# Optimization experiments

Measured on AMD Instinct MI355X. Metric: run time of the kernel, lower is better.

Reference implementation:

```python
import jax, jax.numpy as jnp
import numpy as np

N_NODES = 100000
N_EDGES = 1600000
N_FEAT = 64
HID = 64
HL = 256
N_GRAPHS = 512


def _lin(k, i, o):
    return (jax.random.normal(k, (i, o), jnp.float32) / np.sqrt(i)).astype(jnp.float32)


def setup_inputs() -> dict:
    key = jax.random.key(0)
    ks = jax.random.split(key, 20)
    inp = {
        "x": jax.random.normal(ks[0], (N_NODES, N_FEAT), jnp.float32),
        "edge_index": jax.random.randint(ks[1], (2, N_EDGES), 0, N_NODES),
        "batch": jnp.sort(jax.random.randint(ks[2], (N_NODES,), 0, N_GRAPHS)),
        "T": jax.random.normal(ks[3], (N_GRAPHS, 1), jnp.float32),
    }
    dims = [(N_FEAT, HID), (HID, HID), (HID, HID), (HID, HID)]
    for i, (di, do) in enumerate(dims):
        inp[f"wrel{i}"] = _lin(ks[4 + 3 * i], di, do)
        inp[f"brel{i}"] = jnp.zeros((do,), jnp.float32)
        inp[f"wroot{i}"] = _lin(ks[5 + 3 * i], di, do)
    inp["w1"] = _lin(ks[16], 3 * HID + 1, HL)
    inp["b1"] = jnp.zeros((HL,), jnp.float32)
    inp["w2"] = _lin(ks[17], HL, HL)
    inp["b2"] = jnp.zeros((HL,), jnp.float32)
    inp["w3"] = _lin(ks[18], HL, 1)
    inp["b3"] = jnp.zeros((1,), jnp.float32)
    return inp


def reference(x, edge_index, batch, T,
              wrel0, brel0, wroot0,
              wrel1, brel1, wroot1,
              wrel2, brel2, wroot2,
              wrel3, brel3, wroot3,
              w1, b1, w2, b2, w3, b3):
    src, dst = edge_index[0], edge_index[1]

    def conv(h, wr, br, wq):
        # PyG GraphConv: W_root h_i + W_rel * sum_{j->i} h_j + b_rel
        agg = jax.ops.segment_sum(h[src], dst, num_segments=N_NODES)
        return agg @ wr + br + h @ wq

    h = jax.nn.relu(conv(x, wrel0, brel0, wroot0))
    h = jax.nn.relu(conv(h, wrel1, brel1, wroot1))
    h = jax.nn.relu(conv(h, wrel2, brel2, wroot2))
    h = conv(h, wrel3, brel3, wroot3)  # no relu on conv2 (matches original)

    # global add / mean / max pools over graph ids
    s = jax.ops.segment_sum(h, batch, num_segments=N_GRAPHS)
    cnt = jax.ops.segment_sum(jnp.ones((N_NODES, 1), h.dtype), batch, num_segments=N_GRAPHS)
    mean = s / jnp.maximum(cnt, 1.0)
    mx = jax.ops.segment_max(h, batch, num_segments=N_GRAPHS)
    mx = jnp.where(jnp.isfinite(mx), mx, 0.0)  # empty segments -> 0

    out = jnp.concatenate([mx, mean, s, T], axis=1)  # [G, 3*HID+1]
    o = jax.nn.relu(out @ w1 + b1)
    o = jax.nn.relu(o @ w2 + b2)  # dropout is identity in eval mode
    return o @ w3 + b3
```

## Files before the change

kernel.cpp:

```cpp
#include <hip/hip_runtime.h>
#include <hip/hip_bf16.h>
#include <math.h>

#define N_NODES 100000
#define N_EDGES 1600000
#define N_FEAT 64
#define HID 64
#define HL 256
#define N_GRAPHS 512

#define BUCKET_BITS 7
#define BUCKET_SIZE 128
#define NB ((N_NODES + BUCKET_SIZE - 1) / BUCKET_SIZE)
#define LOFS_W (NB + 1)
#define CAP 3584
#define LREC_CAP 3584
#define EDGES_PER_BLOCK 4096
#define SCAT_BLOCKS ((N_EDGES + EDGES_PER_BLOCK - 1) / EDGES_PER_BLOCK)
#define F2B_BLOCKS (N_NODES * 16 / 256)
#define WPREP_BLOCKS 128
#define ZOFF ((unsigned int)N_NODES * 128u)
#define FUSE_BLOCKS ((N_NODES + 63) / 64)

typedef short vbf8 __attribute__((ext_vector_type(8)));
typedef float vf4 __attribute__((ext_vector_type(4)));
typedef float vf2 __attribute__((ext_vector_type(2)));
typedef unsigned int vu4 __attribute__((ext_vector_type(4)));

__device__ __forceinline__ unsigned short f2b(float f) {
    unsigned int u = __float_as_uint(f);
    return (unsigned short)((u + 0x7FFFu + ((u >> 16) & 1u)) >> 16);
}
__device__ __forceinline__ float b2f(unsigned short u) {
    return __uint_as_float(((unsigned int)u) << 16);
}
__device__ __forceinline__ unsigned pk2(float lo, float hi) {
    float2 f; f.x = lo; f.y = hi;
    __hip_bfloat162 h = __float22bfloat162_rn(f);
    unsigned r;
    __builtin_memcpy(&r, &h, 4);
    return r;
}
__device__ __forceinline__ vf2 bpair(unsigned int d) {
    vf2 r;
    r.x = __uint_as_float(d << 16);
    r.y = __uint_as_float(d & 0xFFFF0000u);
    return r;
}


__global__ __launch_bounds__(256) void k_mega(
        const int* __restrict__ src, const int* __restrict__ dst,
        int* __restrict__ lofs, unsigned int* __restrict__ ebuf,
        const float4* __restrict__ x, uint2* __restrict__ xb,
        const float* __restrict__ wroot0, const float* __restrict__ wrel0,
        const float* __restrict__ wroot1, const float* __restrict__ wrel1,
        const float* __restrict__ wroot2, const float* __restrict__ wrel2,
        const float* __restrict__ wroot3, const float* __restrict__ wrel3,
        unsigned short* __restrict__ wt) {
    __shared__ int lh[NB];
    __shared__ int lsc[256];
    __shared__ unsigned lrec[EDGES_PER_BLOCK];
    int bid = blockIdx.x;
    int t = threadIdx.x;

    if (bid < SCAT_BLOCKS) {
        for (int i = t; i < NB; i += 256) lh[i] = 0;
        __syncthreads();
        int i0 = bid * EDGES_PER_BLOCK;
        int i1 = min(N_EDGES, i0 + EDGES_PER_BLOCK);
        int cnt = i1 - i0;
        for (int i = i0 + t; i < i1; i += 256)
            atomicAdd(&lh[dst[i] >> BUCKET_BITS], 1);
        __syncthreads();
        int v[4];
        int s = 0;
        int base4 = t * 4;
#pragma unroll
        for (int j = 0; j < 4; j++) {
            v[j] = (base4 + j < NB) ? lh[base4 + j] : 0;
            s += v[j];
        }
        lsc[t] = s;
        __syncthreads();
        for (int off = 1; off < 256; off <<= 1) {
            int xx = lsc[t];
            int y = (t >= off) ? lsc[t - off] : 0;
            __syncthreads();
            lsc[t] = xx + y;
            __syncthreads();
        }
        int run = lsc[t] - s;
        int* lrow = lofs + (size_t)bid * LOFS_W;
#pragma unroll
        for (int j = 0; j < 4; j++) {
            int b = base4 + j;
            if (b < NB) {
                lrow[b] = run;
                lh[b] = run;
            }
            run += v[j];
        }
        if (t == 255) lrow[NB] = cnt;
        __syncthreads();
        for (int i = i0 + t; i < i1; i += 256) {
            int sN = src[i], d = dst[i];
            int b = d >> BUCKET_BITS;
            int p = atomicAdd(&lh[b], 1);
            lrec[p] = ((unsigned)sN << 7) | (unsigned)(d & 127);
        }
        __syncthreads();
        unsigned* eb = ebuf + (size_t)bid * EDGES_PER_BLOCK;
        for (int j = t; j < cnt; j += 256) eb[j] = lrec[j];
    } else if (bid < SCAT_BLOCKS + F2B_BLOCKS) {
        int i = (bid - SCAT_BLOCKS) * 256 + t;
        if (i < N_NODES * 16) {
            float4 v = x[i];
            uint2 o;
            o.x = pk2(v.x, v.y);
            o.y = pk2(v.z, v.w);
            xb[i] = o;
        }
    } else {
        int gi = (bid - SCAT_BLOCKS - F2B_BLOCKS) * 256 + t;
        if (gi < 4 * 64 * 128) {
            int layer = gi >> 13;
            int i = gi & 8191;
            int nn = i >> 7, k = i & 127;
            const float* wr = (layer == 0) ? wroot0 : (layer == 1) ? wroot1
                             : (layer == 2) ? wroot2 : wroot3;
            const float* wl = (layer == 0) ? wrel0 : (layer == 1) ? wrel1
                             : (layer == 2) ? wrel2 : wrel3;
            float v = (k < 64) ? wr[k * 64 + nn] : wl[(k - 64) * 64 + nn];
            wt[gi] = f2b(v);
        }
    }
}


__global__ __launch_bounds__(256) void k_fscatter2(
        const unsigned int* __restrict__ ebuf, const int* __restrict__ lofs,
        int2* __restrict__ re, unsigned int* __restrict__ soff,
        unsigned short* __restrict__ hbA, unsigned short* __restrict__ hbB, int n) {
    __shared__ int rcnt[512];
    __shared__ int rbase[512];
    __shared__ int rpre[512];
    __shared__ int tsc[256];
    __shared__ unsigned lrec[LREC_CAP];
    __shared__ int lcnt[BUCKET_SIZE];
    __shared__ int sc[BUCKET_SIZE];
    __shared__ int cur[BUCKET_SIZE];
    int b = blockIdx.x;
    int n0 = b * BUCKET_SIZE;
    int t = threadIdx.x;
    if (b == 0 && t < 16) {
        uint4 z = make_uint4(0u, 0u, 0u, 0u);
        unsigned short* hp = (t < 8) ? hbA : hbB;
        ((uint4*)(hp + (size_t)N_NODES * 64))[t & 7] = z;
    }
    for (int blk = t; blk < 512; blk += 256) {
        int c = 0, ba = 0;
        if (blk < SCAT_BLOCKS) {
            const int* lr = lofs + (size_t)blk * LOFS_W + b;
            ba = lr[0];
            c = lr[1] - ba;
        }
        rcnt[blk] = c;
        rbase[blk] = ba;
    }
    __syncthreads();
    int c0 = rcnt[2 * t], c1 = rcnt[2 * t + 1];
    tsc[t] = c0 + c1;
    __syncthreads();
    for (int off = 1; off < 256; off <<= 1) {
        int xx = tsc[t];
        int y = (t >= off) ? tsc[t - off] : 0;
        __syncthreads();
        tsc[t] = xx + y;
        __syncthreads();
    }
    int ex = tsc[t] - (c0 + c1);
    rpre[2 * t] = ex;
    rpre[2 * t + 1] = ex + c0;
    __syncthreads();
    int cb = tsc[255];
    for (int blk = t; blk < SCAT_BLOCKS; blk += 256) {
        int c = rcnt[blk];
        int dsto = rpre[blk];
        const unsigned* sp = ebuf + (size_t)blk * EDGES_PER_BLOCK + rbase[blk];
        for (int j = 0; j < c; j++) lrec[dsto + j] = sp[j];
    }
    if (t < BUCKET_SIZE) lcnt[t] = 0;
    __syncthreads();
    for (int r = t; r < cb; r += 256)
        atomicAdd(&lcnt[lrec[r] & 127u], 1);
    __syncthreads();
    int v = 0, pcnt = 0;
    if (t < BUCKET_SIZE) {
        v = lcnt[t];
        pcnt = (v + 7) & ~7;
        sc[t] = pcnt;
    }
    __syncthreads();
    for (int off = 1; off < BUCKET_SIZE; off <<= 1) {
        int xx = 0;
        if (t < BUCKET_SIZE) {
            xx = sc[t];
            if (t >= off) xx += sc[t - off];
        }
        __syncthreads();
        if (t < BUCKET_SIZE) sc[t] = xx;
        __syncthreads();
    }
    if (t < BUCKET_SIZE) {
        int start = b * CAP + sc[t] - pcnt;
        if (n0 + t < n) re[n0 + t] = make_int2(start, start + v);
        cur[t] = start;
        for (int z = start + v; z < start + pcnt; z++) soff[z] = ZOFF;
    }
    __syncthreads();
    for (int r = t; r < cb; r += 256) {
        unsigned rec = lrec[r];
        int p = atomicAdd(&cur[rec & 127u], 1);
        soff[p] = rec & ~127u;
    }
}


template <int RELU>
__global__ __launch_bounds__(512) void k_layer(
    const unsigned short* __restrict__ hb,
    const unsigned short* __restrict__ wt, const float* __restrict__ brel,
    unsigned short* __restrict__ hbout,
    const int2* __restrict__ re, const unsigned int* __restrict__ soff, int n) {
    __shared__ float scx[4][16 * 68];
    __shared__ unsigned int agg_lds[64][32];

    int tid = threadIdx.x;
    int w = tid >> 6, l = tid & 63;
    int r0 = blockIdx.x * 64;

    {
        int g = l >> 3;
        int sl = l & 7;
        int nl = w * 8 + g;
        int i = r0 + nl;
        int ii = min(i, n - 1);
        int2 bd = re[ii];
        int e0 = bd.x;
        int cnt = (i < n) ? (bd.y - bd.x) : 0;
        int pc4 = (cnt + 3) & ~3;
        const char* base = (const char*)hb + sl * 16;

        vf2 A[4], B[4];
#pragma unroll
        for (int f = 0; f < 4; f++) { A[f] = (vf2){0.f, 0.f}; B[f] = (vf2){0.f, 0.f}; }

        for (int it = 0; it < pc4; it += 4) {
            vu4 ov = __builtin_nontemporal_load((const vu4*)(soff + e0 + it));
            uint4 d0 = *(const uint4*)(base + ov.x);
            uint4 d1 = *(const uint4*)(base + ov.y);
            uint4 d2 = *(const uint4*)(base + ov.z);
            uint4 d3 = *(const uint4*)(base + ov.w);
            A[0] += bpair(d0.x); A[1] += bpair(d0.y);
            A[2] += bpair(d0.z); A[3] += bpair(d0.w);
            B[0] += bpair(d1.x); B[1] += bpair(d1.y);
            B[2] += bpair(d1.z); B[3] += bpair(d1.w);
            A[0] += bpair(d2.x); A[1] += bpair(d2.y);
            A[2] += bpair(d2.z); A[3] += bpair(d2.w);
            B[0] += bpair(d3.x); B[1] += bpair(d3.y);
            B[2] += bpair(d3.z); B[3] += bpair(d3.w);
        }

        vf2 s0 = A[0] + B[0];
        vf2 s1 = A[1] + B[1];
        vf2 s2 = A[2] + B[2];
        vf2 s3 = A[3] + B[3];
        uint4 o;
        o.x = pk2(s0.x, s0.y);
        o.y = pk2(s1.x, s1.y);
        o.z = pk2(s2.x, s2.y);
        o.w = pk2(s3.x, s3.y);
        int c16 = sl ^ (nl & 7);
        *(uint4*)&agg_lds[nl][c16 * 4] = o;
    }
    __syncthreads();

    if (w < 4) {
        int lm = l & 15, q = l >> 4;
        int row = w * 16 + lm;
        int arow = r0 + row;
        if (arow >= n) arow = n - 1;
        const unsigned short* ah = hb + (size_t)arow * 64 + q * 8;
        vbf8 afr[4];
        afr[0] = *(const vbf8*)(ah);
        afr[1] = *(const vbf8*)(ah + 32);
        afr[2] = *(const vbf8*)&agg_lds[row][((q) ^ (lm & 7)) * 4];
        afr[3] = *(const vbf8*)&agg_lds[row][((q + 4) ^ (lm & 7)) * 4];

        vf4 acc[4];
#pragma unroll
        for (int t = 0; t < 4; t++) acc[t] = (vf4){0.f, 0.f, 0.f, 0.f};

#pragma unroll
        for (int t = 0; t < 4; t++) {
            const unsigned short* wrow = wt + (size_t)(t * 16 + lm) * 128 + q * 8;
#pragma unroll
            for (int s = 0; s < 4; s++) {
                vbf8 bfr = *(const vbf8*)(wrow + s * 32);
                acc[t] = __builtin_amdgcn_mfma_f32_16x16x32_bf16(afr[s], bfr, acc[t], 0, 0, 0);
            }
        }

        float* sw_ = scx[w];
#pragma unroll
        for (int t = 0; t < 4; t++) {
            float b = brel[t * 16 + lm];
#pragma unroll
            for (int i = 0; i < 4; i++) {
                float v = acc[t][i] + b;
                if (RELU) v = fmaxf(v, 0.f);
                sw_[(q * 4 + i) * 68 + t * 16 + lm] = v;
            }
        }
        int rr = l >> 2, cs = l & 3;
        int node = r0 + w * 16 + rr;
        if (node < n) {
            const float* rp = sw_ + rr * 68 + cs * 16;
            float4 v0 = *(const float4*)(rp);
            float4 v1 = *(const float4*)(rp + 4);
            float4 v2 = *(const float4*)(rp + 8);
            float4 v3 = *(const float4*)(rp + 12);
            vu4 o0, o1;
            o0.x = pk2(v0.x, v0.y);
            o0.y = pk2(v0.z, v0.w);
            o0.z = pk2(v1.x, v1.y);
            o0.w = pk2(v1.z, v1.w);
            o1.x = pk2(v2.x, v2.y);
            o1.y = pk2(v2.z, v2.w);
            o1.z = pk2(v3.x, v3.y);
            o1.w = pk2(v3.z, v3.w);
            vu4* op = (vu4*)(hbout + (size_t)node * 64 + cs * 16);
            __builtin_nontemporal_store(o0, op);
            __builtin_nontemporal_store(o1, op + 1);
        }
    }
}


__global__ __launch_bounds__(256) void k_poolmlp(
    const unsigned short* __restrict__ hb, const int* __restrict__ batch,
    const float* __restrict__ T, const float* __restrict__ w1,
    const float* __restrict__ b1, const float* __restrict__ w2,
    const float* __restrict__ b2, const float* __restrict__ w3,
    const float* __restrict__ b3, float* __restrict__ out, int n) {
    __shared__ float psum[4][64];
    __shared__ float pmax[4][64];
    __shared__ float sin_[200];
    __shared__ float so1[256];
    __shared__ float red[256];
    int g = blockIdx.x, t = threadIdx.x;
    int l = t & 63, c = t >> 6;

    int lo = 0, hi = n;
    while (lo < hi) { int m = (lo + hi) >> 1; if (batch[m] < g) lo = m + 1; else hi = m; }
    int s0 = lo;
    int lo2 = s0, hi2 = n;
    while (lo2 < hi2) { int m = (lo2 + hi2) >> 1; if (batch[m] < g + 1) lo2 = m + 1; else hi2 = m; }
    int s1 = lo2;

    float sa0 = 0.f, sa1 = 0.f, sa2 = 0.f, sa3 = 0.f;
    float ma0 = -INFINITY, ma1 = -INFINITY, ma2 = -INFINITY, ma3 = -INFINITY;
    int nn = s0 + c;
    for (; nn + 12 < s1; nn += 16) {
        float v0 = b2f(hb[(size_t)nn * 64 + l]);
        float v1 = b2f(hb[(size_t)(nn + 4) * 64 + l]);
        float v2 = b2f(hb[(size_t)(nn + 8) * 64 + l]);
        float v3 = b2f(hb[(size_t)(nn + 12) * 64 + l]);
        sa0 += v0; sa1 += v1; sa2 += v2; sa3 += v3;
        ma0 = fmaxf(ma0, v0); ma1 = fmaxf(ma1, v1);
        ma2 = fmaxf(ma2, v2); ma3 = fmaxf(ma3, v3);
    }
    for (; nn < s1; nn += 4) {
        float v = b2f(hb[(size_t)nn * 64 + l]);
        sa0 += v;
        ma0 = fmaxf(ma0, v);
    }
    psum[c][l] = (sa0 + sa1) + (sa2 + sa3);
    pmax[c][l] = fmaxf(fmaxf(ma0, ma1), fmaxf(ma2, ma3));
    __syncthreads();
    if (t < 64) {
        float s = (psum[0][t] + psum[1][t]) + (psum[2][t] + psum[3][t]);
        float mx = fmaxf(fmaxf(pmax[0][t], pmax[1][t]), fmaxf(pmax[2][t], pmax[3][t]));
        int cnt = s1 - s0;
        float mean = s / fmaxf((float)cnt, 1.f);
        if (cnt == 0) mx = 0.f;
        sin_[t] = mx;
        sin_[64 + t] = mean;
        sin_[128 + t] = s;
        if (t == 0) {
            sin_[192] = T[g];
#pragma unroll
            for (int z = 193; z < 200; z++) sin_[z] = 0.f;
        }
    }
    __syncthreads();

    float a = b1[t];
    {
        float wv[8];
        for (int k = 0; k < 192; k += 8) {
#pragma unroll
            for (int u = 0; u < 8; u++) wv[u] = w1[(k + u) * 256 + t];
#pragma unroll
            for (int u = 0; u < 8; u++) a += sin_[k + u] * wv[u];
        }
        a += sin_[192] * w1[192 * 256 + t];
    }
    a = fmaxf(a, 0.f);
    so1[t] = a;
    __syncthreads();

    float a2 = b2[t];
    {
        float wv[8];
        for (int k = 0; k < 256; k += 8) {
#pragma unroll
            for (int u = 0; u < 8; u++) wv[u] = w2[(k + u) * 256 + t];
#pragma unroll
            for (int u = 0; u < 8; u++) a2 += so1[k + u] * wv[u];
        }
    }
    a2 = fmaxf(a2, 0.f);
    red[t] = a2 * w3[t];
    __syncthreads();
    for (int s = 128; s > 0; s >>= 1) {
        if (t < s) red[t] += red[t + s];
        __syncthreads();
    }
    if (t == 0) out[g] = red[0] + b3[0];
}

extern "C" void kernel_launch(void* const* d_in, const int* in_sizes, int n_in,
                              void* d_out, int out_size, void* d_ws, size_t ws_size,
                              hipStream_t stream) {
    const int N = N_NODES, E = N_EDGES, G = N_GRAPHS;

    const float* x = (const float*)d_in[0];
    const int* ei = (const int*)d_in[1];
    const int* batch = (const int*)d_in[2];
    const float* T = (const float*)d_in[3];
    const float* wrel[4] = {(const float*)d_in[4], (const float*)d_in[7],
                            (const float*)d_in[10], (const float*)d_in[13]};
    const float* brel[4] = {(const float*)d_in[5], (const float*)d_in[8],
                            (const float*)d_in[11], (const float*)d_in[14]};
    const float* wroot[4] = {(const float*)d_in[6], (const float*)d_in[9],
                             (const float*)d_in[12], (const float*)d_in[15]};
    const float* w1 = (const float*)d_in[16];
    const float* b1 = (const float*)d_in[17];
    const float* w2 = (const float*)d_in[18];
    const float* b2 = (const float*)d_in[19];
    const float* w3 = (const float*)d_in[20];
    const float* b3 = (const float*)d_in[21];
    float* out = (float*)d_out;

    const int* esrc = ei;
    const int* edst = ei + E;

    char* ws = (char*)d_ws;
    size_t off = 0;
    auto alloc = [&](size_t bytes) {
        size_t r = off;
        off = (off + bytes + 255) & ~(size_t)255;
        return r;
    };
    int* lofs = (int*)(ws + alloc((size_t)SCAT_BLOCKS * LOFS_W * 4));
    int2* re = (int2*)(ws + alloc((size_t)N * 8));
    unsigned int* soff = (unsigned int*)(ws + alloc((size_t)NB * CAP * 4));
    unsigned int* ebuf = (unsigned int*)(ws + alloc((size_t)SCAT_BLOCKS * EDGES_PER_BLOCK * 4));
    unsigned short* hbA = (unsigned short*)(ws + alloc((size_t)N * 64 * 2 + 128));
    unsigned short* hbB = (unsigned short*)(ws + alloc((size_t)N * 64 * 2 + 128));
    unsigned short* wt = (unsigned short*)(ws + alloc((size_t)4 * 64 * 128 * 2));

    k_mega<<<SCAT_BLOCKS + F2B_BLOCKS + WPREP_BLOCKS, 256, 0, stream>>>(
        esrc, edst, lofs, ebuf, (const float4*)x, (uint2*)hbA,
        wroot[0], wrel[0], wroot[1], wrel[1],
        wroot[2], wrel[2], wroot[3], wrel[3], wt);
    k_fscatter2<<<NB, 256, 0, stream>>>(ebuf, lofs, re, soff, hbA, hbB, N);

    k_layer<1><<<FUSE_BLOCKS, 512, 0, stream>>>(hbA, wt + 0 * 8192, brel[0], hbB, re, soff, N);
    k_layer<1><<<FUSE_BLOCKS, 512, 0, stream>>>(hbB, wt + 1 * 8192, brel[1], hbA, re, soff, N);
    k_layer<1><<<FUSE_BLOCKS, 512, 0, stream>>>(hbA, wt + 2 * 8192, brel[2], hbB, re, soff, N);
    k_layer<0><<<FUSE_BLOCKS, 512, 0, stream>>>(hbB, wt + 3 * 8192, brel[3], hbA, re, soff, N);

    k_poolmlp<<<G, 256, 0, stream>>>(hbA, batch, T, w1, b1, w2, b2, w3, b3, out, N);
}
```

Baseline: 344.5 us.

## Replace two-pass bucketed CSR build with global-atomic histogram and scatter

Swaps the block-local bucket sort (per-block histograms, prefix offsets, ebuf staging, per-bucket regather) for a simpler CSR build: zero a degree array, count destinations with global atomics, prefix-sum per bucket to get row starts, then scatter sources with global atomic cursors. This removes the ebuf round trip and the serial per-block copy loops in the old fscatter, but adds two kernel launches and 3.2M global atomics on contended addresses. It also drops the nontemporal hint on the soff loads in the layer kernel. Edge order within each row now depends on atomic ordering, so float summation order can vary between runs.

```diff
diff --git a/kernel.cpp b/kernel.cpp
--- a/kernel.cpp
+++ b/kernel.cpp
@@ -12,13 +12,12 @@
 #define BUCKET_BITS 7
 #define BUCKET_SIZE 128
 #define NB ((N_NODES + BUCKET_SIZE - 1) / BUCKET_SIZE)
-#define LOFS_W (NB + 1)
 #define CAP 3584
-#define LREC_CAP 3584
-#define EDGES_PER_BLOCK 4096
-#define SCAT_BLOCKS ((N_EDGES + EDGES_PER_BLOCK - 1) / EDGES_PER_BLOCK)
 #define F2B_BLOCKS (N_NODES * 16 / 256)
 #define WPREP_BLOCKS 128
+#define HIST_BLOCKS 512
+#define SCAT3_BLOCKS 1024
+#define ZERO_BLOCKS ((NB * BUCKET_SIZE + 255) / 256)
 #define ZOFF ((unsigned int)N_NODES * 128u)
 #define FUSE_BLOCKS ((N_NODES + 63) / 64)
 
@@ -49,71 +48,28 @@
 }
 
 
-__global__ __launch_bounds__(256) void k_mega(
-        const int* __restrict__ src, const int* __restrict__ dst,
-        int* __restrict__ lofs, unsigned int* __restrict__ ebuf,
+__global__ __launch_bounds__(256) void k_zero(int* __restrict__ deg) {
+    int i = blockIdx.x * 256 + threadIdx.x;
+    if (i < NB * BUCKET_SIZE) deg[i] = 0;
+}
+
+
+__global__ __launch_bounds__(256) void k_hist(
+        const int* __restrict__ dst, int* __restrict__ deg,
         const float4* __restrict__ x, uint2* __restrict__ xb,
         const float* __restrict__ wroot0, const float* __restrict__ wrel0,
         const float* __restrict__ wroot1, const float* __restrict__ wrel1,
         const float* __restrict__ wroot2, const float* __restrict__ wrel2,
         const float* __restrict__ wroot3, const float* __restrict__ wrel3,
         unsigned short* __restrict__ wt) {
-    __shared__ int lh[NB];
-    __shared__ int lsc[256];
-    __shared__ unsigned lrec[EDGES_PER_BLOCK];
     int bid = blockIdx.x;
     int t = threadIdx.x;
-
-    if (bid < SCAT_BLOCKS) {
-        for (int i = t; i < NB; i += 256) lh[i] = 0;
-        __syncthreads();
-        int i0 = bid * EDGES_PER_BLOCK;
-        int i1 = min(N_EDGES, i0 + EDGES_PER_BLOCK);
-        int cnt = i1 - i0;
-        for (int i = i0 + t; i < i1; i += 256)
-            atomicAdd(&lh[dst[i] >> BUCKET_BITS], 1);
-        __syncthreads();
-        int v[4];
-        int s = 0;
-        int base4 = t * 4;
-#pragma unroll
-        for (int j = 0; j < 4; j++) {
-            v[j] = (base4 + j < NB) ? lh[base4 + j] : 0;
-            s += v[j];
-        }
-        lsc[t] = s;
-        __syncthreads();
-        for (int off = 1; off < 256; off <<= 1) {
-            int xx = lsc[t];
-            int y = (t >= off) ? lsc[t - off] : 0;
-            __syncthreads();
-            lsc[t] = xx + y;
-            __syncthreads();
-        }
-        int run = lsc[t] - s;
-        int* lrow = lofs + (size_t)bid * LOFS_W;
-#pragma unroll
-        for (int j = 0; j < 4; j++) {
-            int b = base4 + j;
-            if (b < NB) {
-                lrow[b] = run;
-                lh[b] = run;
-            }
-            run += v[j];
-        }
-        if (t == 255) lrow[NB] = cnt;
-        __syncthreads();
-        for (int i = i0 + t; i < i1; i += 256) {
-            int sN = src[i], d = dst[i];
-            int b = d >> BUCKET_BITS;
-            int p = atomicAdd(&lh[b], 1);
-            lrec[p] = ((unsigned)sN << 7) | (unsigned)(d & 127);
-        }
-        __syncthreads();
-        unsigned* eb = ebuf + (size_t)bid * EDGES_PER_BLOCK;
-        for (int j = t; j < cnt; j += 256) eb[j] = lrec[j];
-    } else if (bid < SCAT_BLOCKS + F2B_BLOCKS) {
-        int i = (bid - SCAT_BLOCKS) * 256 + t;
+    if (bid < HIST_BLOCKS) {
+        const int total = HIST_BLOCKS * 256;
+        for (int i = bid * 256 + t; i < N_EDGES; i += total)
+            atomicAdd(&deg[dst[i]], 1);
+    } else if (bid < HIST_BLOCKS + F2B_BLOCKS) {
+        int i = (bid - HIST_BLOCKS) * 256 + t;
         if (i < N_NODES * 16) {
             float4 v = x[i];
             uint2 o;
@@ -122,7 +78,7 @@
             xb[i] = o;
         }
     } else {
-        int gi = (bid - SCAT_BLOCKS - F2B_BLOCKS) * 256 + t;
+        int gi = (bid - HIST_BLOCKS - F2B_BLOCKS) * 256 + t;
         if (gi < 4 * 64 * 128) {
             int layer = gi >> 13;
             int i = gi & 8191;
@@ -138,18 +94,11 @@
 }
 
 
-__global__ __launch_bounds__(256) void k_fscatter2(
-        const unsigned int* __restrict__ ebuf, const int* __restrict__ lofs,
-        int2* __restrict__ re, unsigned int* __restrict__ soff,
+__global__ __launch_bounds__(128) void k_prep2(
+        const int* __restrict__ deg, int2* __restrict__ re,
+        unsigned int* __restrict__ soff, int* __restrict__ cur,
         unsigned short* __restrict__ hbA, unsigned short* __restrict__ hbB, int n) {
-    __shared__ int rcnt[512];
-    __shared__ int rbase[512];
-    __shared__ int rpre[512];
-    __shared__ int tsc[256];
-    __shared__ unsigned lrec[LREC_CAP];
-    __shared__ int lcnt[BUCKET_SIZE];
     __shared__ int sc[BUCKET_SIZE];
-    __shared__ int cur[BUCKET_SIZE];
     int b = blockIdx.x;
     int n0 = b * BUCKET_SIZE;
     int t = threadIdx.x;
@@ -158,71 +107,34 @@
         unsigned short* hp = (t < 8) ? hbA : hbB;
         ((uint4*)(hp + (size_t)N_NODES * 64))[t & 7] = z;
     }
-    for (int blk = t; blk < 512; blk += 256) {
-        int c = 0, ba = 0;
-        if (blk < SCAT_BLOCKS) {
-            const int* lr = lofs + (size_t)blk * LOFS_W + b;
-            ba = lr[0];
-            c = lr[1] - ba;
-        }
-        rcnt[blk] = c;
-        rbase[blk] = ba;
-    }
-    __syncthreads();
-    int c0 = rcnt[2 * t], c1 = rcnt[2 * t + 1];
-    tsc[t] = c0 + c1;
-    __syncthreads();
-    for (int off = 1; off < 256; off <<= 1) {
-        int xx = tsc[t];
-        int y = (t >= off) ? tsc[t - off] : 0;
+    int v = (n0 + t < n) ? deg[n0 + t] : 0;
+    int pcnt = (v + 7) & ~7;
+    sc[t] = pcnt;
+    __syncthreads();
+    for (int off = 1; off < BUCKET_SIZE; off <<= 1) {
+        int xx = sc[t];
+        if (t >= off) xx += sc[t - off];
         __syncthreads();
-        tsc[t] = xx + y;
+        sc[t] = xx;
         __syncthreads();
     }
-    int ex = tsc[t] - (c0 + c1);
-    rpre[2 * t] = ex;
-    rpre[2 * t + 1] = ex + c0;
-    __syncthreads();
-    int cb = tsc[255];
-    for (int blk = t; blk < SCAT_BLOCKS; blk += 256) {
-        int c = rcnt[blk];
-        int dsto = rpre[blk];
-        const unsigned* sp = ebuf + (size_t)blk * EDGES_PER_BLOCK + rbase[blk];
-        for (int j = 0; j < c; j++) lrec[dsto + j] = sp[j];
-    }
-    if (t < BUCKET_SIZE) lcnt[t] = 0;
-    __syncthreads();
-    for (int r = t; r < cb; r += 256)
-        atomicAdd(&lcnt[lrec[r] & 127u], 1);
-    __syncthreads();
-    int v = 0, pcnt = 0;
-    if (t < BUCKET_SIZE) {
-        v = lcnt[t];
-        pcnt = (v + 7) & ~7;
-        sc[t] = pcnt;
-    }
-    __syncthreads();
-    for (int off = 1; off < BUCKET_SIZE; off <<= 1) {
-        int xx = 0;
-        if (t < BUCKET_SIZE) {
-            xx = sc[t];
-            if (t >= off) xx += sc[t - off];
-        }
-        __syncthreads();
-        if (t < BUCKET_SIZE) sc[t] = xx;
-        __syncthreads();
-    }
-    if (t < BUCKET_SIZE) {
-        int start = b * CAP + sc[t] - pcnt;
-        if (n0 + t < n) re[n0 + t] = make_int2(start, start + v);
-        cur[t] = start;
-        for (int z = start + v; z < start + pcnt; z++) soff[z] = ZOFF;
-    }
-    __syncthreads();
-    for (int r = t; r < cb; r += 256) {
-        unsigned rec = lrec[r];
-        int p = atomicAdd(&cur[rec & 127u], 1);
-        soff[p] = rec & ~127u;
+    int start = b * CAP + sc[t] - pcnt;
+    if (n0 + t < n) {
+        re[n0 + t] = make_int2(start, start + v);
+        cur[n0 + t] = start;
+    }
+    for (int z = start + v; z < start + pcnt; z++) soff[z] = ZOFF;
+}
+
+
+__global__ __launch_bounds__(256) void k_scat(
+        const int* __restrict__ src, const int* __restrict__ dst,
+        int* __restrict__ cur, unsigned int* __restrict__ soff) {
+    const int total = SCAT3_BLOCKS * 256;
+    for (int i = blockIdx.x * 256 + threadIdx.x; i < N_EDGES; i += total) {
+        int s = src[i], d = dst[i];
+        int p = atomicAdd(&cur[d], 1);
+        soff[p] = (unsigned)s << 7;
     }
 }
 
@@ -257,7 +169,7 @@
         for (int f = 0; f < 4; f++) { A[f] = (vf2){0.f, 0.f}; B[f] = (vf2){0.f, 0.f}; }
 
         for (int it = 0; it < pc4; it += 4) {
-            vu4 ov = __builtin_nontemporal_load((const vu4*)(soff + e0 + it));
+            vu4 ov = *(const vu4*)(soff + e0 + it);
             uint4 d0 = *(const uint4*)(base + ov.x);
             uint4 d1 = *(const uint4*)(base + ov.y);
             uint4 d2 = *(const uint4*)(base + ov.z);
@@ -474,19 +386,21 @@
         off = (off + bytes + 255) & ~(size_t)255;
         return r;
     };
-    int* lofs = (int*)(ws + alloc((size_t)SCAT_BLOCKS * LOFS_W * 4));
+    int* deg = (int*)(ws + alloc((size_t)NB * BUCKET_SIZE * 4));
+    int* cur = (int*)(ws + alloc((size_t)NB * BUCKET_SIZE * 4));
     int2* re = (int2*)(ws + alloc((size_t)N * 8));
     unsigned int* soff = (unsigned int*)(ws + alloc((size_t)NB * CAP * 4));
-    unsigned int* ebuf = (unsigned int*)(ws + alloc((size_t)SCAT_BLOCKS * EDGES_PER_BLOCK * 4));
     unsigned short* hbA = (unsigned short*)(ws + alloc((size_t)N * 64 * 2 + 128));
     unsigned short* hbB = (unsigned short*)(ws + alloc((size_t)N * 64 * 2 + 128));
     unsigned short* wt = (unsigned short*)(ws + alloc((size_t)4 * 64 * 128 * 2));
 
-    k_mega<<<SCAT_BLOCKS + F2B_BLOCKS + WPREP_BLOCKS, 256, 0, stream>>>(
-        esrc, edst, lofs, ebuf, (const float4*)x, (uint2*)hbA,
+    k_zero<<<ZERO_BLOCKS, 256, 0, stream>>>(deg);
+    k_hist<<<HIST_BLOCKS + F2B_BLOCKS + WPREP_BLOCKS, 256, 0, stream>>>(
+        edst, deg, (const float4*)x, (uint2*)hbA,
         wroot[0], wrel[0], wroot[1], wrel[1],
         wroot[2], wrel[2], wroot[3], wrel[3], wt);
-    k_fscatter2<<<NB, 256, 0, stream>>>(ebuf, lofs, re, soff, hbA, hbB, N);
+    k_prep2<<<NB, 128, 0, stream>>>(deg, re, soff, cur, hbA, hbB, N);
+    k_scat<<<SCAT3_BLOCKS, 256, 0, stream>>>(esrc, edst, cur, soff);
 
     k_layer<1><<<FUSE_BLOCKS, 512, 0, stream>>>(hbA, wt + 0 * 8192, brel[0], hbB, re, soff, N);
     k_layer<1><<<FUSE_BLOCKS, 512, 0, stream>>>(hbB, wt + 1 * 8192, brel[1], hbA, re, soff, N);
```

Result: slower. 503.7 us (+46.2%).
